# Performance work log

Measured on AMD Instinct MI355X. Metric: run time of the kernel, lower is better.

Reference implementation:

```python
import jax, jax.numpy as jnp
import numpy as np

GRID_SIZE = 3
SPLINE_ORDER = 3
N_BASIS = GRID_SIZE + SPLINE_ORDER  # 6


def make_grid(in_features, dtype=jnp.float32):
    # efficient-kan grid buffer: extended uniform knots over grid_range=[-1, 1]
    h = 2.0 / GRID_SIZE
    g = jnp.arange(-SPLINE_ORDER, GRID_SIZE + SPLINE_ORDER + 1, dtype=dtype) * h - 1.0
    return jnp.tile(g[None, :], (in_features, 1))  # (in, G + 2S + 1)


def b_splines(x, grid):
    # x: (N, in), grid: (in, G+2S+1) -> (N, in, G+S) via Cox-de Boor recursion
    xb = x[..., None]
    bases = ((xb >= grid[:, :-1]) & (xb < grid[:, 1:])).astype(x.dtype)
    for k in range(1, SPLINE_ORDER + 1):
        bases = ((xb - grid[:, : -(k + 1)]) / (grid[:, k:-1] - grid[:, : -(k + 1)]) * bases[..., :-1]
                 + (grid[:, k + 1:] - xb) / (grid[:, k + 1:] - grid[:, 1:-k]) * bases[..., 1:])
    return bases


def kan_linear(x, base_w, spline_w, scaler, grid):
    # base path: silu(x) @ W_base^T ; spline path: contraction of basis with scaled spline weights
    base = jax.nn.silu(x) @ base_w.T
    scaled_sw = spline_w * scaler[..., None]  # (out, in, K)
    spl = jnp.einsum('nik,oik->no', b_splines(x, grid), scaled_sw)
    return base + spl


def setup_inputs() -> dict:
    key = jax.random.key(0)
    ks = jax.random.split(key, 7)
    B, C, P, D, H = 8, 8, 128, 256, 1024
    s = 0.05
    return {
        'x': jax.random.normal(ks[0], (B, C, P, D), dtype=jnp.float32),
        'base_w1': s * jax.random.normal(ks[1], (H, D), dtype=jnp.float32),
        'spline_w1': s * jax.random.normal(ks[2], (H, D, N_BASIS), dtype=jnp.float32),
        'scaler1': 1.0 + s * jax.random.normal(ks[3], (H, D), dtype=jnp.float32),
        'base_w2': s * jax.random.normal(ks[4], (D, H), dtype=jnp.float32),
        'spline_w2': s * jax.random.normal(ks[5], (D, H, N_BASIS), dtype=jnp.float32),
        'scaler2': 1.0 + s * jax.random.normal(ks[6], (D, H), dtype=jnp.float32),
    }


def reference(x, base_w1, spline_w1, scaler1, base_w2, spline_w2, scaler2):
    B, C, P, D = x.shape
    H = base_w1.shape[0]
    xf = x.reshape(-1, D)  # KANLinear flattens leading dims to tokens
    g1 = make_grid(D, x.dtype)
    g2 = make_grid(H, x.dtype)
    h = kan_linear(xf, base_w1, spline_w1, scaler1, g1)
    h = jax.nn.gelu(h, approximate=False)  # torch F.gelu default = exact erf
    # dropout is identity in eval / with p used as inference baseline
    y = kan_linear(h, base_w2, spline_w2, scaler2, g2)
    return y.reshape(B, C, P, D)
```

## Files before the change

### kernel.cpp

```cpp
#include <hip/hip_runtime.h>
#include <hip/hip_bf16.h>
#include <math.h>


typedef __attribute__((ext_vector_type(8))) short bf16x8;
typedef __attribute__((ext_vector_type(4))) float f32x4;

#define TOKENS 8192
#define D_IN   256
#define D_HID  1024

__device__ __forceinline__ void kan_features(float x, float f[8]) {
    f[0] = x * __builtin_amdgcn_rcpf(1.0f + __expf(-x));
    const float s = (x + 1.0f) * 1.5f + 3.0f;
    const float cf = floorf(s);
    const float u = s - cf;
    const int c = (int)cf;
    const float u2 = u * u, u3 = u2 * u;
    const float k6 = 1.0f / 6.0f;
    const float v3 = u3 * k6;
    const float v2 = (-3.0f * u3 + 3.0f * u2 + 3.0f * u + 1.0f) * k6;
    const float v1 = (3.0f * u3 - 6.0f * u2 + 4.0f) * k6;
    const float w1 = 1.0f - u;
    const float v0 = w1 * w1 * w1 * k6;
    const bool in = (s >= 0.0f) && (s < 9.0f);
#pragma unroll
    for (int j = 0; j < 6; ++j) {
        int d = c - j;
        float bv = (d == 0) ? v3 : (d == 1) ? v2 : (d == 2) ? v1 : (d == 3) ? v0 : 0.0f;
        f[1 + j] = in ? bv : 0.0f;
    }
    f[7] = 0.0f;
}

__device__ __forceinline__ void features_to_bf16(const float f[8], __hip_bfloat16 fb[8]) {
#pragma unroll
    for (int j = 0; j < 8; ++j) fb[j] = __float2bfloat16(f[j]);
}

__global__ void init_fused(const float* __restrict__ X, __hip_bfloat16* __restrict__ F,
                           const float* __restrict__ bw1, const float* __restrict__ sw1,
                           const float* __restrict__ sc1, __hip_bfloat16* __restrict__ W1,
                           const float* __restrict__ bw2, const float* __restrict__ sw2,
                           const float* __restrict__ sc2, __hip_bfloat16* __restrict__ W2f) {
    const int b = blockIdx.x;
    if (b < 8192) {
        int idx = b * 256 + threadIdx.x;
        float f[8];
        kan_features(X[idx], f);
        __hip_bfloat16 fb[8];
        features_to_bf16(f, fb);
        *(bf16x8*)&F[(size_t)idx * 8] = *(bf16x8*)fb;
        return;
    }
    const bool w1 = (b < 9216);
    int idx = (w1 ? (b - 8192) : (b - 9216)) * 256 + threadIdx.x;
    const float* bw = w1 ? bw1 : bw2;
    const float* sw = w1 ? sw1 : sw2;
    const float* sc = w1 ? sc1 : sc2;
    float scl = sc[idx];
    __hip_bfloat16 row[8];
    row[0] = __float2bfloat16(bw[idx]);
#pragma unroll
    for (int j = 0; j < 6; ++j)
        row[1 + j] = __float2bfloat16(sw[idx * 6 + j] * scl);
    row[7] = __float2bfloat16(0.0f);
    if (w1) {
        *(bf16x8*)&W1[(size_t)idx * 8] = *(bf16x8*)row;
    } else {
        int o = idx >> 10, i = idx & 1023;
        *(bf16x8*)&W2f[(size_t)(i >> 2) * 8192 + o * 32 + (i & 3) * 8] = *(bf16x8*)row;
    }
}

#define GLL(src, dst) __builtin_amdgcn_global_load_lds(                         \
    (const __attribute__((address_space(1))) void*)(src),                       \
    (__attribute__((address_space(3))) void*)(dst), 16, 0, 0)

__global__ __launch_bounds__(256, 2)
void kan_gemm1(const __hip_bfloat16* __restrict__ A,
               const __hip_bfloat16* __restrict__ W,
               float* __restrict__ H) {
    constexpr int K = D_IN * 8;
    constexpr int NT = K / 64;
    __shared__ __hip_bfloat16 Al[2][128 * 64];
    __shared__ __hip_bfloat16 Bl[2][128 * 64];

    const int tid = threadIdx.x;
    const int wid = tid >> 6, lane = tid & 63;
    const int wm = wid >> 1, wn = wid & 1;
    const int lr = lane & 15, lg = lane >> 4;
    const int n0 = blockIdx.x * 128, o0 = blockIdx.y * 128;

    int srow[4], sslot[4];
#pragma unroll
    for (int p = 0; p < 4; ++p) {
        int item = tid + p * 256;
        srow[p] = item >> 3;
        sslot[p] = (item & 7) ^ (srow[p] & 7);
    }
    int aoff[2][4], boff[2][4];
#pragma unroll
    for (int ks = 0; ks < 2; ++ks)
#pragma unroll
        for (int f = 0; f < 4; ++f) {
            int ar = wm * 64 + f * 16 + lr;
            int br = wn * 64 + f * 16 + lr;
            aoff[ks][f] = ar * 64 + (((ks * 4 + lg) ^ (ar & 7)) * 8);
            boff[ks][f] = br * 64 + (((ks * 4 + lg) ^ (br & 7)) * 8);
        }

    f32x4 acc[4][4] = {};

#define STG1(buf, kt)                                                           \
    do {                                                                        \
        _Pragma("unroll")                                                       \
        for (int p = 0; p < 4; ++p) {                                           \
            GLL(A + (size_t)(n0 + srow[p]) * K + (kt) * 64 + sslot[p] * 8,      \
                &Al[buf][(tid + p * 256) * 8]);                                 \
            GLL(W + (size_t)(o0 + srow[p]) * K + (kt) * 64 + sslot[p] * 8,      \
                &Bl[buf][(tid + p * 256) * 8]);                                 \
        }                                                                       \
    } while (0)

    STG1(0, 0);
    STG1(1, 1);
    for (int t = 0; t < NT; ++t) {
        const int cur = t & 1;
        asm volatile("s_waitcnt vmcnt(8)" ::: "memory");
        __builtin_amdgcn_s_barrier();
        __builtin_amdgcn_sched_barrier(0);
        __builtin_amdgcn_s_setprio(1);
#pragma unroll
        for (int ks = 0; ks < 2; ++ks) {
            bf16x8 af[4], bfr[4];
#pragma unroll
            for (int f = 0; f < 4; ++f) af[f] = *(const bf16x8*)&Al[cur][aoff[ks][f]];
#pragma unroll
            for (int f = 0; f < 4; ++f) bfr[f] = *(const bf16x8*)&Bl[cur][boff[ks][f]];
#pragma unroll
            for (int fm = 0; fm < 4; ++fm)
#pragma unroll
                for (int fn = 0; fn < 4; ++fn)
                    acc[fm][fn] = __builtin_amdgcn_mfma_f32_16x16x32_bf16(
                        af[fm], bfr[fn], acc[fm][fn], 0, 0, 0);
        }
        __builtin_amdgcn_s_setprio(0);
        asm volatile("s_waitcnt lgkmcnt(0)" ::: "memory");
        __builtin_amdgcn_s_barrier();
        __builtin_amdgcn_sched_barrier(0);
        const int kn = (t + 2 < NT) ? t + 2 : NT - 1;
        STG1(cur, kn);
    }
#undef STG1
#pragma unroll
    for (int fm = 0; fm < 4; ++fm) {
#pragma unroll
        for (int fn = 0; fn < 4; ++fn) {
            int col = o0 + wn * 64 + fn * 16 + lr;
#pragma unroll
            for (int r = 0; r < 4; ++r) {
                int row = n0 + wm * 64 + fm * 16 + lg * 4 + r;
                float v = acc[fm][fn][r];
                H[(size_t)row * D_HID + col] = 0.5f * v * (1.0f + erff(v * 0.70710678118f));
            }
        }
    }
}

__global__ __launch_bounds__(256, 3)
void kan_gemm2(const float* __restrict__ H,
               const __hip_bfloat16* __restrict__ W2f,
               float* __restrict__ P) {
    constexpr int OUT = D_IN, KD = D_HID * 8;
    constexpr int NTT = KD / 64;
    __shared__ __hip_bfloat16 Al[2][64 * 64];

    const int tid = threadIdx.x;
    const int wid = tid >> 6, lane = tid & 63;
    const int lr = lane & 15, lg = lane >> 4;
    const int n0 = blockIdx.x * 64;

    const int per = NTT / 8;
    const int ks0 = blockIdx.z * per, ks1 = ks0 + per;

    const int ar0 = tid >> 3, ac = tid & 7;
    const float* hp0 = H + (size_t)(n0 + ar0) * D_HID + ac;
    const float* hp1 = H + (size_t)(n0 + ar0 + 32) * D_HID + ac;
    const int aw0 = ar0 * 64 + ((ac ^ (ar0 & 7)) * 8);
    const int aw1 = (ar0 + 32) * 64 + ((ac ^ ((ar0 + 32) & 7)) * 8);

    int bcol[4];
#pragma unroll
    for (int f = 0; f < 4; ++f)
        bcol[f] = (wid * 64 + f * 16 + lr) * 32 + lg * 8;

    int aoff[2][4];
#pragma unroll
    for (int ks = 0; ks < 2; ++ks)
#pragma unroll
        for (int f = 0; f < 4; ++f) {
            int ar = f * 16 + lr;
            aoff[ks][f] = ar * 64 + (((ks * 4 + lg) ^ (ar & 7)) * 8);
        }

    f32x4 acc[4][4] = {};

#define FEAT(buf, h0, h1)                                                       \
    do {                                                                        \
        float ff[8]; __hip_bfloat16 fb[8];                                      \
        kan_features(h0, ff); features_to_bf16(ff, fb);                         \
        *(bf16x8*)&Al[buf][aw0] = *(bf16x8*)fb;                                 \
        kan_features(h1, ff); features_to_bf16(ff, fb);                         \
        *(bf16x8*)&Al[buf][aw1] = *(bf16x8*)fb;                                 \
    } while (0)

#define SUB(T, b, nb, DO_STAGE)                                                 \
    do {                                                                        \
        bf16x8 bw[2][4];                                                        \
        _Pragma("unroll")                                                       \
        for (int ks = 0; ks < 2; ++ks)                                          \
            _Pragma("unroll")                                                   \
            for (int f = 0; f < 4; ++f)                                         \
                bw[ks][f] = *(const bf16x8*)&W2f[(size_t)((T) * 2 + ks) * 8192  \
                                                 + bcol[f]];                    \
        if (DO_STAGE) {                                                         \
            FEAT(nb, hA, hB);                                                   \
            int hn = ((T) + 2 < ks1) ? (T) + 2 : ks1 - 1;                       \
            hA = hp0[(size_t)hn * 8];                                           \
            hB = hp1[(size_t)hn * 8];                                           \
        }                                                                       \
        asm volatile("s_waitcnt lgkmcnt(0)" ::: "memory");                      \
        __builtin_amdgcn_sched_barrier(0);                                      \
        __builtin_amdgcn_s_barrier();                                           \
        __builtin_amdgcn_s_setprio(1);                                          \
        _Pragma("unroll")                                                       \
        for (int ks = 0; ks < 2; ++ks) {                                        \
            bf16x8 af[4];                                                       \
            _Pragma("unroll")                                                   \
            for (int f = 0; f < 4; ++f)                                         \
                af[f] = *(const bf16x8*)&Al[b][aoff[ks][f]];                    \
            _Pragma("unroll")                                                   \
            for (int fm = 0; fm < 4; ++fm)                                      \
                _Pragma("unroll")                                               \
                for (int fn = 0; fn < 4; ++fn)                                  \
                    acc[fm][fn] = __builtin_amdgcn_mfma_f32_16x16x32_bf16(      \
                        af[fm], bw[ks][fn], acc[fm][fn], 0, 0, 0);              \
        }                                                                       \
        __builtin_amdgcn_s_setprio(0);                                          \
        __builtin_amdgcn_s_barrier();                                           \
    } while (0)

    {
        float h0 = hp0[(size_t)ks0 * 8];
        float h1 = hp1[(size_t)ks0 * 8];
        FEAT(0, h0, h1);
    }
    float hA = hp0[(size_t)(ks0 + 1) * 8];
    float hB = hp1[(size_t)(ks0 + 1) * 8];

    for (int t = ks0; t < ks1; t += 2) {
        SUB(t, 0, 1, 1);
        SUB(t + 1, 1, 0, (t + 2 < ks1));
    }
#undef SUB
#undef FEAT

    float* Pl = (float*)Al;
    const size_t zoff = (size_t)blockIdx.z * TOKENS * OUT;
#pragma unroll
    for (int q = 0; q < 4; ++q) {
        __syncthreads();
        if (wid == q) {
#pragma unroll
            for (int fm = 0; fm < 4; ++fm)
#pragma unroll
                for (int fn = 0; fn < 4; ++fn)
#pragma unroll
                    for (int r = 0; r < 4; ++r)
                        Pl[(fm * 16 + lg * 4 + r) * 64 + fn * 16 + lr] = acc[fm][fn][r];
        }
        __syncthreads();
#pragma unroll
        for (int p = 0; p < 4; ++p) {
            int v = tid + p * 256;
            int row = v >> 4, cv = (v & 15) * 4;
            *(f32x4*)&P[zoff + (size_t)(n0 + row) * OUT + q * 64 + cv] =
                *(const f32x4*)&Pl[row * 64 + cv];
        }
    }
}

__global__ void reduce_split(const float* __restrict__ P, float* __restrict__ out,
                             int nvec) {
    int i = blockIdx.x * 256 + threadIdx.x;
    if (i >= nvec) return;
    const f32x4* Pv = (const f32x4*)P;
    f32x4 s = Pv[i];
#pragma unroll
    for (int z = 1; z < 8; ++z) s += Pv[(size_t)z * nvec + i];
    ((f32x4*)out)[i] = s;
}

extern "C" void kernel_launch(void* const* d_in, const int* in_sizes, int n_in,
                              void* d_out, int out_size, void* d_ws, size_t ws_size,
                              hipStream_t stream) {
    const float* x   = (const float*)d_in[0];
    const float* bw1 = (const float*)d_in[1];
    const float* sw1 = (const float*)d_in[2];
    const float* sc1 = (const float*)d_in[3];
    const float* bw2 = (const float*)d_in[4];
    const float* sw2 = (const float*)d_in[5];
    const float* sc2 = (const float*)d_in[6];
    float* out = (float*)d_out;

    char* ws = (char*)d_ws;
    __hip_bfloat16* W1  = (__hip_bfloat16*)ws;
    __hip_bfloat16* W2f = (__hip_bfloat16*)(ws + (4ull << 20));
    __hip_bfloat16* F1  = (__hip_bfloat16*)(ws + (8ull << 20));
    float*          Hb  = (float*)(ws + (40ull << 20));
    float*          Pp  = (float*)(ws + (72ull << 20));

    if (ws_size < (136ull << 20)) return;

    init_fused<<<10240, 256, 0, stream>>>(x, F1, bw1, sw1, sc1, W1, bw2, sw2, sc2, W2f);

    kan_gemm1<<<dim3(TOKENS / 128, D_HID / 128), 256, 0, stream>>>(F1, W1, Hb);

    kan_gemm2<<<dim3(TOKENS / 64, 1, 8), 256, 0, stream>>>(Hb, W2f, Pp);

    const int nvec = TOKENS * D_IN / 4;
    reduce_split<<<(nvec + 255) / 256, 256, 0, stream>>>(Pp, out, nvec);
}
```

Measured before the change: 148.1 us.

## Split gemm2 into single-wave blocks computing spline features in registers

Kernel gemm2 now runs one 64-thread wave per block, and the output columns are spread over a new grid y dimension. Each wave computes the B-spline/SiLU features directly into MFMA A-fragments in registers, so the shared-memory feature staging and the per-tile barriers are gone. The cost is that each feature is recomputed by each of the 4 column blocks, giving about 4x the feature math and H reads. The kernel also loses the shared-memory reuse across waves, and the number of blocks grows fourfold.

```diff
diff --git a/kernel.cpp b/kernel.cpp
--- a/kernel.cpp
+++ b/kernel.cpp
@@ -168,124 +168,84 @@
     }
 }
 
-__global__ __launch_bounds__(256, 3)
+__global__ __launch_bounds__(64, 3)
 void kan_gemm2(const float* __restrict__ H,
                const __hip_bfloat16* __restrict__ W2f,
                float* __restrict__ P) {
-    constexpr int OUT = D_IN, KD = D_HID * 8;
-    constexpr int NTT = KD / 64;
-    __shared__ __hip_bfloat16 Al[2][64 * 64];
-
-    const int tid = threadIdx.x;
-    const int wid = tid >> 6, lane = tid & 63;
+    constexpr int OUT = D_IN;
+    const int lane = threadIdx.x;
     const int lr = lane & 15, lg = lane >> 4;
     const int n0 = blockIdx.x * 64;
-
-    const int per = NTT / 8;
-    const int ks0 = blockIdx.z * per, ks1 = ks0 + per;
-
-    const int ar0 = tid >> 3, ac = tid & 7;
-    const float* hp0 = H + (size_t)(n0 + ar0) * D_HID + ac;
-    const float* hp1 = H + (size_t)(n0 + ar0 + 32) * D_HID + ac;
-    const int aw0 = ar0 * 64 + ((ac ^ (ar0 & 7)) * 8);
-    const int aw1 = (ar0 + 32) * 64 + ((ac ^ ((ar0 + 32) & 7)) * 8);
-
+    const int by = blockIdx.y;
+    const int ks0 = blockIdx.z * 16, ks1 = ks0 + 16;
+
+    __shared__ float Pl[32 * 64];
+
+    const float* hrow = H + (size_t)(n0 + lr) * D_HID + lg;
+    const __hip_bfloat16* wp = W2f + (size_t)ks0 * 2 * 8192;
     int bcol[4];
 #pragma unroll
-    for (int f = 0; f < 4; ++f)
-        bcol[f] = (wid * 64 + f * 16 + lr) * 32 + lg * 8;
-
-    int aoff[2][4];
-#pragma unroll
-    for (int ks = 0; ks < 2; ++ks)
-#pragma unroll
-        for (int f = 0; f < 4; ++f) {
-            int ar = f * 16 + lr;
-            aoff[ks][f] = ar * 64 + (((ks * 4 + lg) ^ (ar & 7)) * 8);
-        }
+    for (int f = 0; f < 4; ++f) bcol[f] = (by * 64 + f * 16 + lr) * 32 + lg * 8;
 
     f32x4 acc[4][4] = {};
-
-#define FEAT(buf, h0, h1)                                                       \
+    float hA[8], hB[8];
+
+#define LOADH(d, T)                                                             \
     do {                                                                        \
-        float ff[8]; __hip_bfloat16 fb[8];                                      \
-        kan_features(h0, ff); features_to_bf16(ff, fb);                         \
-        *(bf16x8*)&Al[buf][aw0] = *(bf16x8*)fb;                                 \
-        kan_features(h1, ff); features_to_bf16(ff, fb);                         \
-        *(bf16x8*)&Al[buf][aw1] = *(bf16x8*)fb;                                 \
+        _Pragma("unroll") for (int f = 0; f < 4; ++f)                           \
+        _Pragma("unroll") for (int ks = 0; ks < 2; ++ks)                        \
+            d[f * 2 + ks] = hrow[f * 16 * D_HID + (T) * 8 + ks * 4];            \
     } while (0)
 
-#define SUB(T, b, nb, DO_STAGE)                                                 \
+#define TILE(T, hc, hn, DO)                                                     \
     do {                                                                        \
         bf16x8 bw[2][4];                                                        \
-        _Pragma("unroll")                                                       \
-        for (int ks = 0; ks < 2; ++ks)                                          \
-            _Pragma("unroll")                                                   \
-            for (int f = 0; f < 4; ++f)                                         \
-                bw[ks][f] = *(const bf16x8*)&W2f[(size_t)((T) * 2 + ks) * 8192  \
-                                                 + bcol[f]];                    \
-        if (DO_STAGE) {                                                         \
-            FEAT(nb, hA, hB);                                                   \
-            int hn = ((T) + 2 < ks1) ? (T) + 2 : ks1 - 1;                       \
-            hA = hp0[(size_t)hn * 8];                                           \
-            hB = hp1[(size_t)hn * 8];                                           \
+        _Pragma("unroll") for (int ks = 0; ks < 2; ++ks)                        \
+        _Pragma("unroll") for (int f = 0; f < 4; ++f)                           \
+            bw[ks][f] = *(const bf16x8*)&wp[(size_t)(((T) - ks0) * 2 + ks) * 8192 \
+                                             + bcol[f]];                        \
+        if (DO) LOADH(hn, (T) + 1);                                             \
+        _Pragma("unroll") for (int ks = 0; ks < 2; ++ks) {                      \
+            bf16x8 af[4];                                                       \
+            _Pragma("unroll") for (int f = 0; f < 4; ++f) {                     \
+                float ff[8]; __hip_bfloat16 fb[8];                              \
+                kan_features(hc[f * 2 + ks], ff);                               \
+                features_to_bf16(ff, fb);                                       \
+                af[f] = *(bf16x8*)fb;                                           \
+            }                                                                   \
+            _Pragma("unroll") for (int fm = 0; fm < 4; ++fm)                    \
+            _Pragma("unroll") for (int fn = 0; fn < 4; ++fn)                    \
+                acc[fm][fn] = __builtin_amdgcn_mfma_f32_16x16x32_bf16(          \
+                    af[fm], bw[ks][fn], acc[fm][fn], 0, 0, 0);                  \
         }                                                                       \
-        asm volatile("s_waitcnt lgkmcnt(0)" ::: "memory");                      \
-        __builtin_amdgcn_sched_barrier(0);                                      \
-        __builtin_amdgcn_s_barrier();                                           \
-        __builtin_amdgcn_s_setprio(1);                                          \
-        _Pragma("unroll")                                                       \
-        for (int ks = 0; ks < 2; ++ks) {                                        \
-            bf16x8 af[4];                                                       \
-            _Pragma("unroll")                                                   \
-            for (int f = 0; f < 4; ++f)                                         \
-                af[f] = *(const bf16x8*)&Al[b][aoff[ks][f]];                    \
-            _Pragma("unroll")                                                   \
-            for (int fm = 0; fm < 4; ++fm)                                      \
-                _Pragma("unroll")                                               \
-                for (int fn = 0; fn < 4; ++fn)                                  \
-                    acc[fm][fn] = __builtin_amdgcn_mfma_f32_16x16x32_bf16(      \
-                        af[fm], bw[ks][fn], acc[fm][fn], 0, 0, 0);              \
-        }                                                                       \
-        __builtin_amdgcn_s_setprio(0);                                          \
-        __builtin_amdgcn_s_barrier();                                           \
     } while (0)
 
-    {
-        float h0 = hp0[(size_t)ks0 * 8];
-        float h1 = hp1[(size_t)ks0 * 8];
-        FEAT(0, h0, h1);
-    }
-    float hA = hp0[(size_t)(ks0 + 1) * 8];
-    float hB = hp1[(size_t)(ks0 + 1) * 8];
-
+    LOADH(hA, ks0);
     for (int t = ks0; t < ks1; t += 2) {
-        SUB(t, 0, 1, 1);
-        SUB(t + 1, 1, 0, (t + 2 < ks1));
-    }
-#undef SUB
-#undef FEAT
-
-    float* Pl = (float*)Al;
+        TILE(t, hA, hB, 1);
+        TILE(t + 1, hB, hA, (t + 2 < ks1));
+    }
+#undef TILE
+#undef LOADH
+
     const size_t zoff = (size_t)blockIdx.z * TOKENS * OUT;
 #pragma unroll
-    for (int q = 0; q < 4; ++q) {
+    for (int h = 0; h < 2; ++h) {
         __syncthreads();
-        if (wid == q) {
-#pragma unroll
-            for (int fm = 0; fm < 4; ++fm)
-#pragma unroll
-                for (int fn = 0; fn < 4; ++fn)
-#pragma unroll
-                    for (int r = 0; r < 4; ++r)
-                        Pl[(fm * 16 + lg * 4 + r) * 64 + fn * 16 + lr] = acc[fm][fn][r];
-        }
+#pragma unroll
+        for (int fp = 0; fp < 2; ++fp)
+#pragma unroll
+            for (int fn = 0; fn < 4; ++fn)
+#pragma unroll
+                for (int r = 0; r < 4; ++r)
+                    Pl[(fp * 16 + lg * 4 + r) * 64 + fn * 16 + lr] =
+                        acc[2 * h + fp][fn][r];
         __syncthreads();
 #pragma unroll
-        for (int p = 0; p < 4; ++p) {
-            int v = tid + p * 256;
+        for (int p = 0; p < 8; ++p) {
+            int v = lane + p * 64;
             int row = v >> 4, cv = (v & 15) * 4;
-            *(f32x4*)&P[zoff + (size_t)(n0 + row) * OUT + q * 64 + cv] =
+            *(f32x4*)&P[zoff + (size_t)(n0 + h * 32 + row) * OUT + by * 64 + cv] =
                 *(const f32x4*)&Pl[row * 64 + cv];
         }
     }
@@ -327,7 +287,7 @@
 
     kan_gemm1<<<dim3(TOKENS / 128, D_HID / 128), 256, 0, stream>>>(F1, W1, Hb);
 
-    kan_gemm2<<<dim3(TOKENS / 64, 1, 8), 256, 0, stream>>>(Hb, W2f, Pp);
+    kan_gemm2<<<dim3(TOKENS / 64, D_IN / 64, 8), 64, 0, stream>>>(Hb, W2f, Pp);
 
     const int nvec = TOKENS * D_IN / 4;
     reduce_split<<<(nvec + 255) / 256, 256, 0, stream>>>(Pp, out, nvec);
```

Measured after the change: 274.0 us. 84.9% more time.
